# Kernel tuning notes

Measured on AMD Instinct MI355X. Metric: run time of the kernel, lower is better.

## Reference

```python
import jax, jax.numpy as jnp
import numpy as np
import math

B, L, S, D, H = 4, 2048, 2048, 1024, 16

def setup_inputs() -> dict:
    key = jax.random.key(0)
    ks = jax.random.split(key, 7)
    s = 0.02
    return {
        "queries": jax.random.normal(ks[0], (B, L, D), jnp.float32),
        "keys": jax.random.normal(ks[1], (B, S, D), jnp.float32),
        "values": jax.random.normal(ks[2], (B, S, D), jnp.float32),
        "Wq": jax.random.normal(ks[3], (D, D), jnp.float32) * s,
        "Wk": jax.random.normal(ks[4], (D, D), jnp.float32) * s,
        "Wv": jax.random.normal(ks[5], (D, D), jnp.float32) * s,
        "Wo": jax.random.normal(ks[6], (D, D), jnp.float32) * s,
    }

def _split_heads(x):
    # [B, T, D] -> [B, H, T, d_head]
    b, t, _ = x.shape
    return x.reshape(b, t, H, D // H).transpose(0, 2, 1, 3)

def reference(queries, keys, values, Wq, Wk, Wv, Wo):
    # torch nn.Linear: y = x @ W.T; dropout is identity (p=0 / eval)
    q = _split_heads(queries @ Wq.T)   # [B,H,L,dh]
    k = _split_heads(keys @ Wk.T)      # [B,H,S,dh]
    v = _split_heads(values @ Wv.T)    # [B,H,S,dh]
    dh = q.shape[-1]
    scores = jnp.einsum('bhld,bhsd->bhls', q, k) / math.sqrt(dh)
    causal = jnp.tril(jnp.ones((L, S), dtype=bool))
    scores = jnp.where(causal, scores, -jnp.inf)
    attn = jax.nn.softmax(scores, axis=-1)
    out = jnp.einsum('bhls,bhsd->bhld', attn, v)   # [B,H,L,dh]
    out = out.transpose(0, 2, 1, 3).reshape(B, L, D)
    return out @ Wo.T
```

## Files before the change

### kernel.cpp

```cpp
#include <hip/hip_runtime.h>
#include <hip/hip_bf16.h>
#include <stdint.h>

typedef __bf16 bf16_t;
typedef __bf16 bf16x4 __attribute__((ext_vector_type(4)));
typedef __bf16 bf16x8 __attribute__((ext_vector_type(8)));
typedef float  f32x4  __attribute__((ext_vector_type(4)));
typedef float  f32x16 __attribute__((ext_vector_type(16)));
typedef unsigned int u32;

#define B_  4
#define L_  2048
#define D_  1024
#define H_  16
#define DH_ 64

__device__ __forceinline__ void async_load16(const bf16_t* g, bf16_t* lds) {
    __builtin_amdgcn_global_load_lds(
        (__attribute__((address_space(1))) void*)g,
        (__attribute__((address_space(3))) void*)lds, 16, 0, 0);
}

__global__ __launch_bounds__(256) void cvt_all(
    const float* __restrict__ a0, const float* __restrict__ a1,
    const float* __restrict__ a2,
    const float* __restrict__ w0, const float* __restrict__ w1,
    const float* __restrict__ w2, const float* __restrict__ w3,
    bf16_t* __restrict__ oa0, bf16_t* __restrict__ oa1, bf16_t* __restrict__ oa2,
    bf16_t* __restrict__ ow0, bf16_t* __restrict__ ow1,
    bf16_t* __restrict__ ow2, bf16_t* __restrict__ ow3)
{
    int i = blockIdx.x * 256 + threadIdx.x;
    const float* src; bf16_t* dst; size_t j;
    if (i < 3 * (1 << 21)) {
        int which = i >> 21;
        src = which == 0 ? a0 : which == 1 ? a1 : a2;
        dst = which == 0 ? oa0 : which == 1 ? oa1 : oa2;
        j = (size_t)(i & ((1 << 21) - 1)) * 4;
    } else {
        int k = i - 3 * (1 << 21);
        int which = k >> 18;
        src = which == 0 ? w0 : which == 1 ? w1 : which == 2 ? w2 : w3;
        dst = which == 0 ? ow0 : which == 1 ? ow1 : which == 2 ? ow2 : ow3;
        j = (size_t)(k & ((1 << 18) - 1)) * 4;
    }
    f32x4 v = *(const f32x4*)(src + j);
    bf16x4 ov;
    ov[0] = (bf16_t)v[0]; ov[1] = (bf16_t)v[1];
    ov[2] = (bf16_t)v[2]; ov[3] = (bf16_t)v[3];
    *(bf16x4*)(dst + j) = ov;
}

__device__ __forceinline__ void stage_ab(
    const bf16_t* __restrict__ A, const bf16_t* __restrict__ Bm,
    bf16_t* lds, int rowBase, int colBase, int k0, int t)
{
    const int wbase = t & ~63;
    #pragma unroll
    for (int sweep = 0; sweep < 4; ++sweep) {
        int c = sweep * 256 + t;
        int r = c >> 3, kc = c & 7;
        int kcs = kc ^ (r & 7);
        async_load16(&A[((size_t)(rowBase + r) << 10) + k0 + kcs * 8],
                     &lds[(sweep * 256 + wbase) * 8]);
        async_load16(&Bm[((size_t)(colBase + r) << 10) + k0 + kcs * 8],
                     &lds[8192 + (sweep * 256 + wbase) * 8]);
    }
}

__device__ __forceinline__ void gemm_bt_body(
    const bf16_t* __restrict__ A, const bf16_t* __restrict__ Bm,
    bf16_t* __restrict__ Cb, float* __restrict__ Cf,
    int mode, bf16_t* lds)
{
    const int t = threadIdx.x;
    const int w = t >> 6, l = t & 63;
    const int l31 = l & 31, hi = l >> 5;
    const int wm = w >> 1, wn = w & 1;
    const int rowBase = blockIdx.y * 128;
    const int colBase = blockIdx.x * 128;

    f32x16 acc[2][2] = {};

    for (int k0 = 0; k0 < 1024; k0 += 64) {
        stage_ab(A, Bm, lds, rowBase, colBase, k0, t);
        __syncthreads();

        #pragma unroll
        for (int ks = 0; ks < 4; ++ks) {
            int g = ks * 2 + hi;
            bf16x8 af[2], bg[2];
            #pragma unroll
            for (int mf = 0; mf < 2; ++mf) {
                int row = wm * 64 + mf * 32 + l31;
                af[mf] = *(const bf16x8*)&lds[row * 64 + ((g ^ (row & 7)) * 8)];
            }
            #pragma unroll
            for (int nf = 0; nf < 2; ++nf) {
                int row = wn * 64 + nf * 32 + l31;
                bg[nf] = *(const bf16x8*)&lds[8192 + row * 64 + ((g ^ (row & 7)) * 8)];
            }
            #pragma unroll
            for (int mf = 0; mf < 2; ++mf)
                #pragma unroll
                for (int nf = 0; nf < 2; ++nf)
                    acc[mf][nf] = __builtin_amdgcn_mfma_f32_32x32x16_bf16(
                        af[mf], bg[nf], acc[mf][nf], 0, 0, 0);
        }
        __syncthreads();
    }

    #pragma unroll
    for (int mf = 0; mf < 2; ++mf)
        #pragma unroll
        for (int nf = 0; nf < 2; ++nf)
            #pragma unroll
            for (int reg = 0; reg < 16; ++reg) {
                int row = rowBase + wm * 64 + mf * 32
                        + (reg & 3) + 8 * (reg >> 2) + 4 * hi;
                int col = colBase + wn * 64 + nf * 32 + l31;
                float v = acc[mf][nf][reg];
                if (mode == 0) {
                    Cb[((size_t)row << 10) + col] = (bf16_t)v;
                } else if (mode == 1) {
                    int b = row >> 11, s = row & 2047;
                    int h = col >> 6,  d = col & 63;
                    Cb[(((size_t)((b * H_ + h) * DH_ + d)) << 11) + s] = (bf16_t)v;
                } else {
                    Cf[((size_t)row << 10) + col] = v;
                }
            }
}

__global__ __launch_bounds__(256) void gemm_bt(
    const bf16_t* __restrict__ A, const bf16_t* __restrict__ Bm,
    bf16_t* __restrict__ Cb, float* __restrict__ Cf, int mode)
{
    __shared__ __align__(16) bf16_t lds[16384];
    gemm_bt_body(A, Bm, Cb, Cf, mode, lds);
}

__global__ __launch_bounds__(256) void gemm_qkv(
    const bf16_t* __restrict__ A0, const bf16_t* __restrict__ B0, bf16_t* __restrict__ C0,
    const bf16_t* __restrict__ A1, const bf16_t* __restrict__ B1, bf16_t* __restrict__ C1,
    const bf16_t* __restrict__ A2, const bf16_t* __restrict__ B2, bf16_t* __restrict__ C2)
{
    __shared__ __align__(16) bf16_t lds[16384];
    const int z = blockIdx.z;
    const bf16_t* A  = z == 0 ? A0 : z == 1 ? A1 : A2;
    const bf16_t* Bm = z == 0 ? B0 : z == 1 ? B1 : B2;
    bf16_t*       C  = z == 0 ? C0 : z == 1 ? C1 : C2;
    gemm_bt_body(A, Bm, C, nullptr, z == 2 ? 1 : 0, lds);
}

__device__ __forceinline__ u32 pack2(float a, float b) {
    union { u32 u; bf16_t h[2]; } p;
    p.h[0] = (bf16_t)a; p.h[1] = (bf16_t)b;
    return p.u;
}

__device__ __forceinline__ void stage_kv(
    const bf16_t* __restrict__ Kw, const bf16_t* __restrict__ Vt,
    bf16_t* kl, bf16_t* vl, int b, int h, int j0, int w, int l)
{
    #pragma unroll
    for (int q2 = 0; q2 < 2; ++q2) {
        int c  = q2 * 256 + w * 64 + l;
        int rr = c >> 3, kc = c & 7;
        int kcs = kc ^ (rr & 7);
        async_load16(&Kw[(size_t)(b * L_ + j0 + rr) * D_ + h * DH_ + kcs * 8],
                     &kl[(q2 * 256 + w * 64) * 8]);
        async_load16(&Vt[((size_t)((b * H_ + h) * DH_ + rr)) * (size_t)L_ + j0 + kcs * 8],
                     &vl[(q2 * 256 + w * 64) * 8]);
    }
}

__global__ __launch_bounds__(256) void attn_fwd(
    const bf16_t* __restrict__ Qw, const bf16_t* __restrict__ Kw,
    const bf16_t* __restrict__ Vt, bf16_t* __restrict__ Ow)
{
    __shared__ __align__(16) bf16_t k_lds[2][4096];
    __shared__ __align__(16) bf16_t v_lds[2][4096];
    __shared__ float l_scr[4][32];

    const int t = threadIdx.x;
    const int w = t >> 6, l = t & 63;
    const int l31 = l & 31, hi = l >> 5;
    const int pr = blockIdx.x;
    const int h = blockIdx.y, b = blockIdx.z;

    #pragma unroll 1
    for (int pass = 0; pass < 2; ++pass) {
        const int qt = pass == 0 ? (15 - pr) : pr;
        const int qrow = qt * 128 + w * 32 + l31;

        bf16x8 bq[4];
        {
            const bf16_t* qp = Qw + (size_t)(b * L_ + qrow) * D_ + h * DH_ + hi * 8;
            #pragma unroll
            for (int kd = 0; kd < 4; ++kd) {
                bq[kd] = *(const bf16x8*)(qp + kd * 16);
                #pragma unroll
                for (int j = 0; j < 8; ++j)
                    bq[kd][j] = (bf16_t)((float)bq[kd][j] * 0.180336880f);
            }
        }

        f32x16 acc0 = {}, acc1 = {};
        float m_i = -1e30f, l_i = 0.f;

        stage_kv(Kw, Vt, k_lds[0], v_lds[0], b, h, 0, w, l);
        __syncthreads();

        const int nkt  = 2 * qt + 2;
        const int wmax = qt * 128 + w * 32 + 31;
        int cur = 0;
        for (int jt = 0; jt < nkt; ++jt) {
            if (jt + 1 < nkt)
                stage_kv(Kw, Vt, k_lds[cur ^ 1], v_lds[cur ^ 1], b, h, (jt + 1) * 64, w, l);

            const int j0 = jt * 64;
            if (j0 <= wmax) {
                f32x16 s0 = {}, s1 = {};
                #pragma unroll
                for (int kd = 0; kd < 4; ++kd) {
                    int sw = ((kd * 2 + hi) ^ (l31 & 7)) * 8;
                    bf16x8 ak0 = *(const bf16x8*)&k_lds[cur][l31 * 64 + sw];
                    bf16x8 ak1 = *(const bf16x8*)&k_lds[cur][(32 + l31) * 64 + sw];
                    s0 = __builtin_amdgcn_mfma_f32_32x32x16_bf16(ak0, bq[kd], s0, 0, 0, 0);
                    s1 = __builtin_amdgcn_mfma_f32_32x32x16_bf16(ak1, bq[kd], s1, 0, 0, 0);
                }

                if (jt >= 2 * qt) {
                    #pragma unroll
                    for (int reg = 0; reg < 16; ++reg) {
                        int row = (reg & 3) + 8 * (reg >> 2) + 4 * hi;
                        if (j0 + row > qrow)      s0[reg] = -1e30f;
                        if (j0 + 32 + row > qrow) s1[reg] = -1e30f;
                    }
                }

                float mt_[16];
                #pragma unroll
                for (int r = 0; r < 16; ++r) mt_[r] = fmaxf(s0[r], s1[r]);
                #pragma unroll
                for (int st = 8; st > 0; st >>= 1)
                    #pragma unroll
                    for (int r = 0; r < st; ++r) mt_[r] = fmaxf(mt_[r], mt_[r + st]);
                float mx = fmaxf(mt_[0], __shfl_xor(mt_[0], 32));

                int grew = !(mx <= m_i + 8.f);
                if (__any(grew)) {
                    float mn = fmaxf(m_i, mx);
                    float alpha = exp2f(m_i - mn);
                    m_i = mn; l_i *= alpha;
                    l_scr[w][l31] = alpha;
                    asm volatile("s_waitcnt lgkmcnt(0)" ::: "memory");
                    #pragma unroll
                    for (int reg = 0; reg < 16; ++reg) {
                        int row = (reg & 3) + 8 * (reg >> 2) + 4 * hi;
                        float a2 = l_scr[w][row];
                        acc0[reg] *= a2; acc1[reg] *= a2;
                    }
                }

                #pragma unroll
                for (int r = 0; r < 16; ++r) s0[r] = exp2f(s0[r] - m_i);
                #pragma unroll
                for (int r = 0; r < 16; ++r) s1[r] = exp2f(s1[r] - m_i);
                float st_[16];
                #pragma unroll
                for (int r = 0; r < 16; ++r) st_[r] = s0[r] + s1[r];
                #pragma unroll
                for (int st = 8; st > 0; st >>= 1)
                    #pragma unroll
                    for (int r = 0; r < st; ++r) st_[r] += st_[r + st];
                l_i += st_[0] + __shfl_xor(st_[0], 32);

                #pragma unroll
                for (int ks = 0; ks < 4; ++ks) {
                    float e0, e1, e2, e3, e4, e5, e6, e7;
                    if (ks == 0)      { e0=s0[0]; e1=s0[1]; e2=s0[2];  e3=s0[3];
                                        e4=s0[4]; e5=s0[5]; e6=s0[6];  e7=s0[7]; }
                    else if (ks == 1) { e0=s0[8]; e1=s0[9]; e2=s0[10]; e3=s0[11];
                                        e4=s0[12];e5=s0[13];e6=s0[14]; e7=s0[15]; }
                    else if (ks == 2) { e0=s1[0]; e1=s1[1]; e2=s1[2];  e3=s1[3];
                                        e4=s1[4]; e5=s1[5]; e6=s1[6];  e7=s1[7]; }
                    else              { e0=s1[8]; e1=s1[9]; e2=s1[10]; e3=s1[11];
                                        e4=s1[12];e5=s1[13];e6=s1[14]; e7=s1[15]; }
                    u32 lo01 = pack2(e0, e1), lo23 = pack2(e2, e3);
                    u32 hi45 = pack2(e4, e5), hi67 = pack2(e6, e7);
                    u32 send0 = hi ? lo01 : hi45;
                    u32 send1 = hi ? lo23 : hi67;
                    u32 recv0 = __shfl_xor(send0, 32);
                    u32 recv1 = __shfl_xor(send1, 32);
                    union { u32 uw[4]; bf16x8 v8; } pu;
                    pu.uw[0] = hi ? recv0 : lo01;
                    pu.uw[1] = hi ? recv1 : lo23;
                    pu.uw[2] = hi ? hi45 : recv0;
                    pu.uw[3] = hi ? hi67 : recv1;

                    int sw = ((ks * 2 + hi) ^ (l31 & 7)) * 8;
                    bf16x8 bv0 = *(const bf16x8*)&v_lds[cur][l31 * 64 + sw];
                    bf16x8 bv1 = *(const bf16x8*)&v_lds[cur][(32 + l31) * 64 + sw];
                    acc0 = __builtin_amdgcn_mfma_f32_32x32x16_bf16(pu.v8, bv0, acc0, 0, 0, 0);
                    acc1 = __builtin_amdgcn_mfma_f32_32x32x16_bf16(pu.v8, bv1, acc1, 0, 0, 0);
                }
            }

            __syncthreads();
            cur ^= 1;
        }

        l_scr[w][l31] = l_i;
        asm volatile("s_waitcnt lgkmcnt(0)" ::: "memory");
        #pragma unroll
        for (int reg = 0; reg < 16; ++reg) {
            int row = (reg & 3) + 8 * (reg >> 2) + 4 * hi;
            float inv = 1.f / l_scr[w][row];
            int grow = qt * 128 + w * 32 + row;
            size_t base = (size_t)(b * L_ + grow) * D_ + h * DH_ + l31;
            Ow[base]      = (bf16_t)(acc0[reg] * inv);
            Ow[base + 32] = (bf16_t)(acc1[reg] * inv);
        }
    }
}

extern "C" void kernel_launch(void* const* d_in, const int* in_sizes, int n_in,
                              void* d_out, int out_size, void* d_ws, size_t ws_size,
                              hipStream_t stream)
{
    const float* queries = (const float*)d_in[0];
    const float* keys    = (const float*)d_in[1];
    const float* values  = (const float*)d_in[2];
    const float* Wq = (const float*)d_in[3];
    const float* Wk = (const float*)d_in[4];
    const float* Wv = (const float*)d_in[5];
    const float* Wo = (const float*)d_in[6];
    float* out = (float*)d_out;

    const size_t SZ = (size_t)B_ * L_ * D_;
    const size_t WZ = (size_t)D_ * D_;
    bf16_t* cbuf  = (bf16_t*)d_ws;
    bf16_t* cWq   = cbuf + SZ;
    bf16_t* cWk   = cWq + WZ;
    bf16_t* cWv   = cWk + WZ;
    bf16_t* cWo   = cWv + WZ;
    bf16_t* q_ws  = cWo + WZ;
    bf16_t* k_ws  = q_ws + SZ;
    bf16_t* vt_ws = k_ws + SZ;
    bf16_t* a_ws  = cbuf;

    bf16_t* ck = (bf16_t*)d_out;
    bf16_t* cv = ck + SZ;

    cvt_all<<<28672, 256, 0, stream>>>(queries, keys, values, Wq, Wk, Wv, Wo,
                                       cbuf, ck, cv, cWq, cWk, cWv, cWo);

    gemm_qkv<<<dim3(D_ / 128, (B_ * L_) / 128, 3), 256, 0, stream>>>(
        cbuf, cWq, q_ws,
        ck,   cWk, k_ws,
        cv,   cWv, vt_ws);

    attn_fwd<<<dim3(8, H_, B_), 256, 0, stream>>>(q_ws, k_ws, vt_ws, a_ws);

    gemm_bt<<<dim3(D_ / 128, (B_ * L_) / 128), 256, 0, stream>>>(
        a_ws, cWo, nullptr, out, 2);
}
```

Before: 366.2 us.

## Remap GEMM block order, split V transpose kernel, permute K rows to skip P shuffles

Reorders GEMM tile assignment so consecutive blocks walk down rows within a column stripe, which is meant to improve L2 reuse of the weight tiles. The strided transposed V store in the QKV GEMM epilogue is replaced by a separate LDS-based transpose kernel with vectorized writes. Staged K rows are permuted so the score fragments already sit in the MFMA A-operand layout, which removes the cross-lane shuffles when packing P for the PV product. In exchange it adds an extra kernel launch and an extra round trip of V through memory, and it reuses buffers.

```diff
diff --git a/kernel.cpp b/kernel.cpp
--- a/kernel.cpp
+++ b/kernel.cpp
@@ -77,8 +77,10 @@
     const int w = t >> 6, l = t & 63;
     const int l31 = l & 31, hi = l >> 5;
     const int wm = w >> 1, wn = w & 1;
-    const int rowBase = blockIdx.y * 128;
-    const int colBase = blockIdx.x * 128;
+    const int f  = blockIdx.x + (blockIdx.y << 3);
+    const int nf = ((f & 7) << 6) + (f >> 3);
+    const int rowBase = (nf >> 3) * 128;
+    const int colBase = (nf & 7) * 128;
 
     f32x16 acc[2][2] = {};
 
@@ -96,16 +98,16 @@
                 af[mf] = *(const bf16x8*)&lds[row * 64 + ((g ^ (row & 7)) * 8)];
             }
             #pragma unroll
-            for (int nf = 0; nf < 2; ++nf) {
-                int row = wn * 64 + nf * 32 + l31;
-                bg[nf] = *(const bf16x8*)&lds[8192 + row * 64 + ((g ^ (row & 7)) * 8)];
+            for (int nfi = 0; nfi < 2; ++nfi) {
+                int row = wn * 64 + nfi * 32 + l31;
+                bg[nfi] = *(const bf16x8*)&lds[8192 + row * 64 + ((g ^ (row & 7)) * 8)];
             }
             #pragma unroll
             for (int mf = 0; mf < 2; ++mf)
                 #pragma unroll
-                for (int nf = 0; nf < 2; ++nf)
-                    acc[mf][nf] = __builtin_amdgcn_mfma_f32_32x32x16_bf16(
-                        af[mf], bg[nf], acc[mf][nf], 0, 0, 0);
+                for (int nfi = 0; nfi < 2; ++nfi)
+                    acc[mf][nfi] = __builtin_amdgcn_mfma_f32_32x32x16_bf16(
+                        af[mf], bg[nfi], acc[mf][nfi], 0, 0, 0);
         }
         __syncthreads();
     }
@@ -113,19 +115,15 @@
     #pragma unroll
     for (int mf = 0; mf < 2; ++mf)
         #pragma unroll
-        for (int nf = 0; nf < 2; ++nf)
+        for (int nfi = 0; nfi < 2; ++nfi)
             #pragma unroll
             for (int reg = 0; reg < 16; ++reg) {
                 int row = rowBase + wm * 64 + mf * 32
                         + (reg & 3) + 8 * (reg >> 2) + 4 * hi;
-                int col = colBase + wn * 64 + nf * 32 + l31;
-                float v = acc[mf][nf][reg];
+                int col = colBase + wn * 64 + nfi * 32 + l31;
+                float v = acc[mf][nfi][reg];
                 if (mode == 0) {
                     Cb[((size_t)row << 10) + col] = (bf16_t)v;
-                } else if (mode == 1) {
-                    int b = row >> 11, s = row & 2047;
-                    int h = col >> 6,  d = col & 63;
-                    Cb[(((size_t)((b * H_ + h) * DH_ + d)) << 11) + s] = (bf16_t)v;
                 } else {
                     Cf[((size_t)row << 10) + col] = v;
                 }
@@ -150,7 +148,36 @@
     const bf16_t* A  = z == 0 ? A0 : z == 1 ? A1 : A2;
     const bf16_t* Bm = z == 0 ? B0 : z == 1 ? B1 : B2;
     bf16_t*       C  = z == 0 ? C0 : z == 1 ? C1 : C2;
-    gemm_bt_body(A, Bm, C, nullptr, z == 2 ? 1 : 0, lds);
+    gemm_bt_body(A, Bm, C, nullptr, 0, lds);
+}
+
+__global__ __launch_bounds__(256) void transpose_v(
+    const bf16_t* __restrict__ Vr, bf16_t* __restrict__ Vt)
+{
+    __shared__ __align__(16) bf16_t T[64][72];
+    const int t = threadIdx.x;
+    const int st = blockIdx.x;
+    const int h = blockIdx.y, b = blockIdx.z;
+
+    #pragma unroll
+    for (int k = 0; k < 2; ++k) {
+        int c = k * 256 + t;
+        int s = c >> 3, dch = c & 7;
+        bf16x8 v = *(const bf16x8*)
+            &Vr[(size_t)(b * L_ + st * 64 + s) * D_ + h * DH_ + dch * 8];
+        #pragma unroll
+        for (int e = 0; e < 8; ++e)
+            T[dch * 8 + e][s] = v[e];
+    }
+    __syncthreads();
+    #pragma unroll
+    for (int k = 0; k < 2; ++k) {
+        int c = k * 256 + t;
+        int d = c >> 3, sch = c & 7;
+        bf16x8 v = *(const bf16x8*)&T[d][sch * 8];
+        *(bf16x8*)&Vt[(((size_t)((b * H_ + h) * DH_ + d)) << 11)
+                      + st * 64 + sch * 8] = v;
+    }
 }
 
 __device__ __forceinline__ u32 pack2(float a, float b) {
@@ -168,7 +195,8 @@
         int c  = q2 * 256 + w * 64 + l;
         int rr = c >> 3, kc = c & 7;
         int kcs = kc ^ (rr & 7);
-        async_load16(&Kw[(size_t)(b * L_ + j0 + rr) * D_ + h * DH_ + kcs * 8],
+        int rs = (rr & ~12) | ((rr & 4) << 1) | ((rr & 8) >> 1);
+        async_load16(&Kw[(size_t)(b * L_ + j0 + rs) * D_ + h * DH_ + kcs * 8],
                      &kl[(q2 * 256 + w * 64) * 8]);
         async_load16(&Vt[((size_t)((b * H_ + h) * DH_ + rr)) * (size_t)L_ + j0 + kcs * 8],
                      &vl[(q2 * 256 + w * 64) * 8]);
@@ -234,9 +262,9 @@
                 if (jt >= 2 * qt) {
                     #pragma unroll
                     for (int reg = 0; reg < 16; ++reg) {
-                        int row = (reg & 3) + 8 * (reg >> 2) + 4 * hi;
-                        if (j0 + row > qrow)      s0[reg] = -1e30f;
-                        if (j0 + 32 + row > qrow) s1[reg] = -1e30f;
+                        int key = (reg & 7) + 8 * hi + 16 * (reg >> 3);
+                        if (j0 + key > qrow)      s0[reg] = -1e30f;
+                        if (j0 + 32 + key > qrow) s1[reg] = -1e30f;
                     }
                 }
 
@@ -277,28 +305,17 @@
                     for (int r = 0; r < st; ++r) st_[r] += st_[r + st];
                 l_i += st_[0] + __shfl_xor(st_[0], 32);
 
+                const float* e0p = (const float*)&s0;
+                const float* e1p = (const float*)&s1;
                 #pragma unroll
                 for (int ks = 0; ks < 4; ++ks) {
-                    float e0, e1, e2, e3, e4, e5, e6, e7;
-                    if (ks == 0)      { e0=s0[0]; e1=s0[1]; e2=s0[2];  e3=s0[3];
-                                        e4=s0[4]; e5=s0[5]; e6=s0[6];  e7=s0[7]; }
-                    else if (ks == 1) { e0=s0[8]; e1=s0[9]; e2=s0[10]; e3=s0[11];
-                                        e4=s0[12];e5=s0[13];e6=s0[14]; e7=s0[15]; }
-                    else if (ks == 2) { e0=s1[0]; e1=s1[1]; e2=s1[2];  e3=s1[3];
-                                        e4=s1[4]; e5=s1[5]; e6=s1[6];  e7=s1[7]; }
-                    else              { e0=s1[8]; e1=s1[9]; e2=s1[10]; e3=s1[11];
-                                        e4=s1[12];e5=s1[13];e6=s1[14]; e7=s1[15]; }
-                    u32 lo01 = pack2(e0, e1), lo23 = pack2(e2, e3);
-                    u32 hi45 = pack2(e4, e5), hi67 = pack2(e6, e7);
-                    u32 send0 = hi ? lo01 : hi45;
-                    u32 send1 = hi ? lo23 : hi67;
-                    u32 recv0 = __shfl_xor(send0, 32);
-                    u32 recv1 = __shfl_xor(send1, 32);
+                    const float* e = (ks < 2) ? e0p : e1p;
+                    const int base = (ks & 1) * 8;
                     union { u32 uw[4]; bf16x8 v8; } pu;
-                    pu.uw[0] = hi ? recv0 : lo01;
-                    pu.uw[1] = hi ? recv1 : lo23;
-                    pu.uw[2] = hi ? hi45 : recv0;
-                    pu.uw[3] = hi ? hi67 : recv1;
+                    pu.uw[0] = pack2(e[base + 0], e[base + 1]);
+                    pu.uw[1] = pack2(e[base + 2], e[base + 3]);
+                    pu.uw[2] = pack2(e[base + 4], e[base + 5]);
+                    pu.uw[3] = pack2(e[base + 6], e[base + 7]);
 
                     int sw = ((ks * 2 + hi) ^ (l31 & 7)) * 8;
                     bf16x8 bv0 = *(const bf16x8*)&v_lds[cur][l31 * 64 + sw];
@@ -349,7 +366,6 @@
     bf16_t* q_ws  = cWo + WZ;
     bf16_t* k_ws  = q_ws + SZ;
     bf16_t* vt_ws = k_ws + SZ;
-    bf16_t* a_ws  = cbuf;
 
     bf16_t* ck = (bf16_t*)d_out;
     bf16_t* cv = ck + SZ;
@@ -357,13 +373,14 @@
     cvt_all<<<28672, 256, 0, stream>>>(queries, keys, values, Wq, Wk, Wv, Wo,
                                        cbuf, ck, cv, cWq, cWk, cWv, cWo);
 
-    gemm_qkv<<<dim3(D_ / 128, (B_ * L_) / 128, 3), 256, 0, stream>>>(
+    gemm_qkv<<<dim3(8, 64, 3), 256, 0, stream>>>(
         cbuf, cWq, q_ws,
         ck,   cWk, k_ws,
         cv,   cWv, vt_ws);
 
-    attn_fwd<<<dim3(8, H_, B_), 256, 0, stream>>>(q_ws, k_ws, vt_ws, a_ws);
-
-    gemm_bt<<<dim3(D_ / 128, (B_ * L_) / 128), 256, 0, stream>>>(
-        a_ws, cWo, nullptr, out, 2);
-}
+    transpose_v<<<dim3(32, H_, B_), 256, 0, stream>>>(vt_ws, cbuf);
+
+    attn_fwd<<<dim3(8, H_, B_), 256, 0, stream>>>(q_ws, k_ws, cbuf, vt_ws);
+
+    gemm_bt<<<dim3(8, 64), 256, 0, stream>>>(vt_ws, cWo, nullptr, out, 2);
+}
```

After: 324.2 us. 11.5% less time.
